# Kernel optimization log

Measured on AMD Instinct MI355X. Metric: run time of the kernel, lower is better.

## Reference

```python
import jax, jax.numpy as jnp
import numpy as np

B, L_I, L_H, L_Q, Hs, Ws, K, A = 256, 2, 150, 10, 128, 128, 40, 5


def _conv(x, w, pad):
    # NCHW conv, stride 1
    return jax.lax.conv_general_dilated(
        x, w, window_strides=(1, 1), padding=[(pad, pad), (pad, pad)],
        dimension_numbers=('NCHW', 'OIHW', 'NCHW'))


def setup_inputs() -> dict:
    key = jax.random.key(0)
    ks = jax.random.split(key, 8)
    return {
        'input_view': jax.random.normal(ks[0], (B, L_I, Hs, Ws), dtype=jnp.float32),
        'coords': jax.random.randint(ks[1], (B, 4), 0, Hs, dtype=jnp.int32),
        'h_w': jax.random.normal(ks[2], (L_H, L_I, 3, 3), dtype=jnp.float32) * 0.05,
        'h_b': jax.random.normal(ks[3], (L_H,), dtype=jnp.float32) * 0.05,
        'r_w': jax.random.normal(ks[4], (1, L_H, 1, 1), dtype=jnp.float32) * 0.05,
        'q_w': jax.random.normal(ks[5], (L_Q, 1, 3, 3), dtype=jnp.float32) * 0.05,
        'w': jax.random.normal(ks[6], (L_Q, 1, 3, 3), dtype=jnp.float32) * 0.05,
        'fc_w': jax.random.normal(ks[7], (A, L_Q), dtype=jnp.float32) * 0.05,
    }


def reference(input_view, coords, h_w, h_b, r_w, q_w, w, fc_w):
    # process_input: h = Conv3x3(input_view), r = Conv1x1(h), q0 = Conv3x3(r)
    h = _conv(input_view, h_w, pad=1) + h_b[None, :, None, None]
    r = _conv(h, r_w, pad=0)                       # [B,1,H,W] reward map
    q = _conv(r, q_w, pad=1)                       # [B,L_Q,H,W]
    v = jnp.max(q, axis=1, keepdims=True)          # [B,1,H,W]

    # value_iteration: k-1 sweeps of eval_q + channel max, then one final eval_q
    wq = jnp.concatenate([q_w, w], axis=1)         # [L_Q,2,3,3]

    def step(_, v):
        q_i = _conv(jnp.concatenate([r, v], axis=1), wq, pad=1)
        return jnp.max(q_i, axis=1, keepdims=True)

    v = jax.lax.fori_loop(0, K - 1, step, v)
    q = _conv(jnp.concatenate([r, v], axis=1), wq, pad=1)  # [B,L_Q,H,W]

    # get_action: gather q at agent state, then fc (no bias)
    sx, sy = coords[:, 0], coords[:, 1]
    q_out = q[jnp.arange(B), :, sx, sy]            # [B,L_Q]
    logits = q_out @ fc_w.T                        # [B,5]
    return logits
```

## Files before the change

kernel.cpp:

```cpp
#include <hip/hip_runtime.h>

#define NBATCH 256
#define LI 2
#define LH 150
#define LQ 10
#define HS 128
#define WSD 128
#define KIT 40
#define AOUT 5

#define LCOLS 132
#define LROWS 130
#define PLANE (LROWS * LCOLS)
#define LDS_DWORDS (2 * PLANE)

#define WSOFF_RPLANES 64
#define WS_NEED_BYTES ((size_t)(WSOFF_RPLANES + NBATCH * PLANE) * 4)

typedef float v2f __attribute__((ext_vector_type(2)));
#define SPLAT(K) ((v2f){(K), (K)})
#define FMA2(A, B, C) __builtin_elementwise_fma((A), (B), (C))

__global__ void prep_weff(const float* __restrict__ h_w,
                          const float* __restrict__ h_b,
                          const float* __restrict__ r_w,
                          float* __restrict__ w_eff) {
  const int t = threadIdx.x;
  if (t < 18) {
    const int i = t / 9, k = t % 9;
    double s = 0.0;
    for (int h = 0; h < LH; ++h)
      s += (double)r_w[h] * (double)h_w[(h * LI + i) * 9 + k];
    w_eff[t] = (float)s;
  } else if (t == 18) {
    double s = 0.0;
    for (int h = 0; h < LH; ++h)
      s += (double)r_w[h] * (double)h_b[h];
    w_eff[18] = (float)s;
  }
}


#define LOAD_PROW(P, R, W)                                                   \
  {                                                                          \
    const float4 b_ = *reinterpret_cast<const float4*>((P) + (R) * LCOLS);   \
    const float2 c_ = *reinterpret_cast<const float2*>((P) + (R) * LCOLS + 4); \
    W[0] = (v2f){b_.x, b_.y};                                                \
    W[1] = (v2f){b_.z, b_.w};                                                \
    W[2] = (v2f){c_.x, c_.y};                                                \
  }

#define TAPROW(KY, WARR, K0, K1, K2)                                         \
    a0 = FMA2(SPLAT(K0), WARR[KY][0], a0);                                   \
    a1 = FMA2(SPLAT(K0), WARR[KY][1], a1);                                   \
    a0.x = __builtin_fmaf((K1), WARR[KY][0].y, a0.x);                        \
    a0.y = __builtin_fmaf((K1), WARR[KY][1].x, a0.y);                        \
    a1.x = __builtin_fmaf((K1), WARR[KY][1].y, a1.x);                        \
    a1.y = __builtin_fmaf((K1), WARR[KY][2].x, a1.y);                        \
    a0 = FMA2(SPLAT(K2), WARR[KY][1], a0);                                   \
    a1 = FMA2(SPLAT(K2), WARR[KY][2], a1);

#define VI_CH(QC, WC, MERGE)                                                 \
  {                                                                          \
    const float* qc = (QC);                                                  \
    const float* wc = (WC);                                                  \
    v2f a0 = SPLAT(qc[0]) * rw[0][0];                                        \
    v2f a1 = SPLAT(qc[0]) * rw[0][1];                                        \
    a0.x = __builtin_fmaf(qc[1], rw[0][0].y, a0.x);                          \
    a0.y = __builtin_fmaf(qc[1], rw[0][1].x, a0.y);                          \
    a1.x = __builtin_fmaf(qc[1], rw[0][1].y, a1.x);                          \
    a1.y = __builtin_fmaf(qc[1], rw[0][2].x, a1.y);                          \
    a0 = FMA2(SPLAT(qc[2]), rw[0][1], a0);                                   \
    a1 = FMA2(SPLAT(qc[2]), rw[0][2], a1);                                   \
    TAPROW(1, rw, qc[3], qc[4], qc[5])                                       \
    TAPROW(2, rw, qc[6], qc[7], qc[8])                                       \
    TAPROW(0, vw, wc[0], wc[1], wc[2])                                       \
    TAPROW(1, vw, wc[3], wc[4], wc[5])                                       \
    TAPROW(2, vw, wc[6], wc[7], wc[8])                                       \
    MERGE                                                                    \
  }

#define VI_CHANNELS                                                          \
    v2f o0, o1;                                                              \
    VI_CH(q_w, w_in, o0 = a0; o1 = a1;)                                      \
    _Pragma("unroll 3")                                                      \
    for (int c = 1; c < LQ; ++c) {                                           \
      VI_CH(q_w + c * 9, w_in + c * 9,                                       \
            o0 = __builtin_elementwise_max(o0, a0);                          \
            o1 = __builtin_elementwise_max(o1, a1);)                         \
    }

#define VI_ROW_L(DY)                                                         \
  {                                                                          \
    VI_CHANNELS                                                              \
    outv[DY][0] = o0; outv[DY][1] = o1;                                      \
  }

#define WIN_SHIFT2(NEXTROW)                                                  \
  {                                                                          \
    _Pragma("unroll")                                                        \
    for (int j = 0; j < 3; ++j) {                                            \
      rw[0][j] = rw[1][j]; rw[1][j] = rw[2][j];                              \
      vw[0][j] = vw[1][j]; vw[1][j] = vw[2][j];                              \
    }                                                                        \
    LOAD_PROW(rp, (NEXTROW), rw[2])                                          \
    LOAD_PROW(vp, (NEXTROW), vw[2])                                          \
  }

#define R_ROW(DY)                                                            \
  {                                                                          \
    v2f a0 = SPLAT(beff);                                                    \
    v2f a1 = a0;                                                             \
    TAPROW(0, rw, w_eff[0], w_eff[1], w_eff[2])                              \
    TAPROW(1, rw, w_eff[3], w_eff[4], w_eff[5])                              \
    TAPROW(2, rw, w_eff[6], w_eff[7], w_eff[8])                              \
    TAPROW(0, vw, w_eff[9], w_eff[10], w_eff[11])                            \
    TAPROW(1, vw, w_eff[12], w_eff[13], w_eff[14])                           \
    TAPROW(2, vw, w_eff[15], w_eff[16], w_eff[17])                           \
    racc[DY][0] = a0; racc[DY][1] = a1;                                      \
  }

#define LOADR(SLOT, R)                                                       \
  {                                                                          \
    const float4 b_ = *reinterpret_cast<const float4*>(rp + (R) * LCOLS);    \
    const float2 c_ = *reinterpret_cast<const float2*>(rp + (R) * LCOLS + 4); \
    rP[SLOT][0] = (v2f){b_.x, b_.y};                                         \
    rP[SLOT][1] = (v2f){b_.z, b_.w};                                         \
    rP[SLOT][2] = (v2f){c_.x, c_.y};                                         \
  }

#define LOADV(SLOT, R)                                                       \
  {                                                                          \
    const float4 b_ = *reinterpret_cast<const float4*>(vp + (R) * LCOLS);    \
    const float2 c_ = *reinterpret_cast<const float2*>(vp + (R) * LCOLS + 4); \
    vE[SLOT][0] = (v2f){b_.x, b_.y};                                         \
    vE[SLOT][1] = (v2f){b_.z, b_.w};                                         \
    vE[SLOT][2] = (v2f){c_.x, c_.y};                                         \
    vO[SLOT][0] = (v2f){b_.y, b_.z};                                         \
    vO[SLOT][1] = (v2f){b_.w, c_.x};                                         \
  }

#define TAP_R(SLOT, K0, K1, K2)                                              \
    a0 = FMA2(SPLAT(K0), rP[SLOT][0], a0);                                   \
    a1 = FMA2(SPLAT(K0), rP[SLOT][1], a1);                                   \
    a0.x = __builtin_fmaf((K1), rP[SLOT][0].y, a0.x);                        \
    a0.y = __builtin_fmaf((K1), rP[SLOT][1].x, a0.y);                        \
    a1.x = __builtin_fmaf((K1), rP[SLOT][1].y, a1.x);                        \
    a1.y = __builtin_fmaf((K1), rP[SLOT][2].x, a1.y);                        \
    a0 = FMA2(SPLAT(K2), rP[SLOT][1], a0);                                   \
    a1 = FMA2(SPLAT(K2), rP[SLOT][2], a1);

#define TAP_V(SLOT, K0, K1, K2)                                              \
    a0 = FMA2(SPLAT(K0), vE[SLOT][0], a0);                                   \
    a1 = FMA2(SPLAT(K0), vE[SLOT][1], a1);                                   \
    a0 = FMA2(SPLAT(K1), vO[SLOT][0], a0);                                   \
    a1 = FMA2(SPLAT(K1), vO[SLOT][1], a1);                                   \
    a0 = FMA2(SPLAT(K2), vE[SLOT][1], a0);                                   \
    a1 = FMA2(SPLAT(K2), vE[SLOT][2], a1);

#define VI_CH3(QC, WC, SA, SB, SC, MERGE)                                    \
  {                                                                          \
    const float* qc = (QC);                                                  \
    const float* wc = (WC);                                                  \
    v2f a0 = SPLAT(qc[0]) * rP[SA][0];                                       \
    v2f a1 = SPLAT(qc[0]) * rP[SA][1];                                       \
    a0.x = __builtin_fmaf(qc[1], rP[SA][0].y, a0.x);                         \
    a0.y = __builtin_fmaf(qc[1], rP[SA][1].x, a0.y);                         \
    a1.x = __builtin_fmaf(qc[1], rP[SA][1].y, a1.x);                         \
    a1.y = __builtin_fmaf(qc[1], rP[SA][2].x, a1.y);                         \
    a0 = FMA2(SPLAT(qc[2]), rP[SA][1], a0);                                  \
    a1 = FMA2(SPLAT(qc[2]), rP[SA][2], a1);                                  \
    TAP_R(SB, qc[3], qc[4], qc[5])                                           \
    TAP_R(SC, qc[6], qc[7], qc[8])                                           \
    TAP_V(SA, wc[0], wc[1], wc[2])                                           \
    TAP_V(SB, wc[3], wc[4], wc[5])                                           \
    TAP_V(SC, wc[6], wc[7], wc[8])                                           \
    MERGE                                                                    \
  }

#define VI_OUT(DY, SA, SB, SC)                                               \
  {                                                                          \
    v2f o0, o1;                                                              \
    VI_CH3(q_w, w_in, SA, SB, SC, o0 = a0; o1 = a1;)                         \
    _Pragma("unroll 3")                                                      \
    for (int c = 1; c < LQ; ++c) {                                           \
      VI_CH3(q_w + c * 9, w_in + c * 9, SA, SB, SC,                          \
             o0 = __builtin_elementwise_max(o0, a0);                         \
             o1 = __builtin_elementwise_max(o1, a1);)                        \
    }                                                                        \
    float* w_ = wr + (DY) * LCOLS;                                           \
    w_[1] = o0.x; w_[2] = o0.y; w_[3] = o1.x; w_[4] = o1.y;                  \
  }

__global__ __launch_bounds__(1024)
__attribute__((amdgpu_waves_per_eu(4, 4)))
void vin_gr(const float* __restrict__ input,
            const int* __restrict__ coords,
            const float* __restrict__ q_w,
            const float* __restrict__ w_in,
            const float* __restrict__ fc_w,
            float* __restrict__ ws,
            float* __restrict__ out) {
  extern __shared__ float lds[];
  float* pA = lds;
  float* pB = lds + PLANE;
  const float* w_eff = ws;
  float* g_r = ws + WSOFF_RPLANES + (size_t)blockIdx.x * PLANE;

  const int b = blockIdx.x;
  const int tid = threadIdx.x;
  const int ty = tid >> 5;
  const int tx = tid & 31;
  const int y0 = ty << 2;
  const int x0 = tx << 2;
  const int nb_base = y0 * LCOLS + x0;
  const int wrow0 = (y0 + 1) * LCOLS + x0;

  for (int i = tid; i < LDS_DWORDS; i += 1024) lds[i] = 0.0f;
  if (tid < LCOLS) { g_r[tid] = 0.0f; g_r[129 * LCOLS + tid] = 0.0f; }
  if (tid >= 256 && tid < 384) {
    const int row = tid - 255;
    g_r[row * LCOLS + 0] = 0.0f;
    g_r[row * LCOLS + 129] = 0.0f;
    g_r[row * LCOLS + 130] = 0.0f;
    g_r[row * LCOLS + 131] = 0.0f;
  }
  __syncthreads();

  const float* in0 = input + (size_t)b * (LI * HS * WSD);
  const float* in1 = in0 + HS * WSD;
  {
    const float4* in40 = (const float4*)in0;
    const float4* in41 = (const float4*)in1;
    for (int i = tid; i < HS * WSD / 4; i += 1024) {
      const int y = i >> 5, x4 = (i & 31) << 2;
      const float4 a = in40[i];
      const float4 c = in41[i];
      float* r_ = pA + (y + 1) * LCOLS + x4;
      float* v_ = pB + (y + 1) * LCOLS + x4;
      r_[1] = a.x; r_[2] = a.y; r_[3] = a.z; r_[4] = a.w;
      v_[1] = c.x; v_[2] = c.y; v_[3] = c.z; v_[4] = c.w;
    }
  }
  __syncthreads();

  {
    const float* rp = pA + nb_base;
    const float* vp = pB + nb_base;
    v2f rw[3][3], vw[3][3], racc[4][2];
    LOAD_PROW(rp, 0, rw[0]) LOAD_PROW(rp, 1, rw[1]) LOAD_PROW(rp, 2, rw[2])
    LOAD_PROW(vp, 0, vw[0]) LOAD_PROW(vp, 1, vw[1]) LOAD_PROW(vp, 2, vw[2])
    const float beff = w_eff[18];
    R_ROW(0) WIN_SHIFT2(3) R_ROW(1) WIN_SHIFT2(4) R_ROW(2) WIN_SHIFT2(5) R_ROW(3)
    __syncthreads();
#pragma unroll
    for (int dy = 0; dy < 4; ++dy) {
      float* g_ = g_r + wrow0 + dy * LCOLS;
      float* v_ = pA + wrow0 + dy * LCOLS;
      g_[1] = racc[dy][0].x; g_[2] = racc[dy][0].y;
      g_[3] = racc[dy][1].x; g_[4] = racc[dy][1].y;
      v_[1] = 0.0f; v_[2] = 0.0f; v_[3] = 0.0f; v_[4] = 0.0f;
    }
  }
  __syncthreads();

  const float* grp = g_r + nb_base;
#pragma unroll 1
  for (int it = 0; it < KIT; ++it) {
    const float* vp = lds + ((it & 1) ? PLANE : 0) + nb_base;
    float* wr = lds + ((it & 1) ? 0 : PLANE) + wrow0;
    const float* rp = grp;
    v2f rP[3][3], vE[3][3], vO[3][2];
    LOADR(0, 0) LOADR(1, 1) LOADR(2, 2)
    LOADV(0, 0) LOADV(1, 1) LOADV(2, 2)
    VI_OUT(0, 0, 1, 2)
    LOADR(0, 3) LOADV(0, 3)
    VI_OUT(1, 1, 2, 0)
    LOADR(1, 4) LOADV(1, 4)
    VI_OUT(2, 2, 0, 1)
    LOADR(2, 5) LOADV(2, 5)
    VI_OUT(3, 0, 1, 2)
    __syncthreads();
  }

  if (tid == 0) {
    const int sx = coords[b * 4 + 0];
    const int sy = coords[b * 4 + 1];
    float qv[LQ];
#pragma unroll 1
    for (int c = 0; c < LQ; ++c) {
      float s = 0.0f;
#pragma unroll
      for (int kk = 0; kk < 9; ++kk) {
        const int ky = kk / 3, kx = kk % 3;
        const int off = (sx + ky) * LCOLS + (sy + kx);
        s = __builtin_fmaf(q_w[c * 9 + kk], g_r[off],
            __builtin_fmaf(w_in[c * 9 + kk], pA[off], s));
      }
      qv[c] = s;
    }
#pragma unroll 1
    for (int a = 0; a < AOUT; ++a) {
      float s = 0.0f;
#pragma unroll
      for (int c = 0; c < LQ; ++c)
        s = __builtin_fmaf(fc_w[a * LQ + c], qv[c], s);
      out[b * AOUT + a] = s;
    }
  }
}

__global__ __launch_bounds__(1024)
__attribute__((amdgpu_waves_per_eu(4, 4)))
void vin_lds(const float* __restrict__ input,
             const int* __restrict__ coords,
             const float* __restrict__ q_w,
             const float* __restrict__ w_in,
             const float* __restrict__ fc_w,
             const float* __restrict__ w_eff,
             float* __restrict__ out) {
  extern __shared__ float lds[];
  float* rplane = lds;
  float* vplane = lds + PLANE;

  const int b = blockIdx.x;
  const int tid = threadIdx.x;
  const int ty = tid >> 5;
  const int tx = tid & 31;
  const int y0 = ty << 2;
  const int x0 = tx << 2;
  const int nb_base = y0 * LCOLS + x0;
  const int wrow0 = (y0 + 1) * LCOLS + x0;

  for (int i = tid; i < LDS_DWORDS; i += 1024) lds[i] = 0.0f;
  __syncthreads();

  const float* in0 = input + (size_t)b * (LI * HS * WSD);
  const float* in1 = in0 + HS * WSD;
  {
    const float4* in40 = (const float4*)in0;
    const float4* in41 = (const float4*)in1;
    for (int i = tid; i < HS * WSD / 4; i += 1024) {
      const int y = i >> 5, x4 = (i & 31) << 2;
      const float4 a = in40[i];
      const float4 c = in41[i];
      float* r_ = rplane + (y + 1) * LCOLS + x4;
      float* v_ = vplane + (y + 1) * LCOLS + x4;
      r_[1] = a.x; r_[2] = a.y; r_[3] = a.z; r_[4] = a.w;
      v_[1] = c.x; v_[2] = c.y; v_[3] = c.z; v_[4] = c.w;
    }
  }
  __syncthreads();

  {
    const float* rp = rplane + nb_base;
    const float* vp = vplane + nb_base;
    v2f rw[3][3], vw[3][3], racc[4][2];
    LOAD_PROW(rp, 0, rw[0]) LOAD_PROW(rp, 1, rw[1]) LOAD_PROW(rp, 2, rw[2])
    LOAD_PROW(vp, 0, vw[0]) LOAD_PROW(vp, 1, vw[1]) LOAD_PROW(vp, 2, vw[2])
    const float beff = w_eff[18];
    R_ROW(0) WIN_SHIFT2(3) R_ROW(1) WIN_SHIFT2(4) R_ROW(2) WIN_SHIFT2(5) R_ROW(3)
    __syncthreads();
#pragma unroll
    for (int dy = 0; dy < 4; ++dy) {
      float* r_ = rplane + wrow0 + dy * LCOLS;
      float* v_ = vplane + wrow0 + dy * LCOLS;
      r_[1] = racc[dy][0].x; r_[2] = racc[dy][0].y;
      r_[3] = racc[dy][1].x; r_[4] = racc[dy][1].y;
      v_[1] = 0.0f; v_[2] = 0.0f; v_[3] = 0.0f; v_[4] = 0.0f;
    }
  }
  __syncthreads();

#pragma unroll 1
  for (int it = 0; it < KIT; ++it) {
    const float* rp = rplane + nb_base;
    const float* vp = vplane + nb_base;
    v2f rw[3][3], vw[3][3], outv[4][2];
    LOAD_PROW(rp, 0, rw[0]) LOAD_PROW(rp, 1, rw[1]) LOAD_PROW(rp, 2, rw[2])
    LOAD_PROW(vp, 0, vw[0]) LOAD_PROW(vp, 1, vw[1]) LOAD_PROW(vp, 2, vw[2])
    VI_ROW_L(0) WIN_SHIFT2(3) VI_ROW_L(1) WIN_SHIFT2(4) VI_ROW_L(2) WIN_SHIFT2(5) VI_ROW_L(3)
    __syncthreads();
#pragma unroll
    for (int dy = 0; dy < 4; ++dy) {
      float* v_ = vplane + wrow0 + dy * LCOLS;
      v_[1] = outv[dy][0].x; v_[2] = outv[dy][0].y;
      v_[3] = outv[dy][1].x; v_[4] = outv[dy][1].y;
    }
    __syncthreads();
  }

  if (tid == 0) {
    const int sx = coords[b * 4 + 0];
    const int sy = coords[b * 4 + 1];
    float qv[LQ];
#pragma unroll 1
    for (int c = 0; c < LQ; ++c) {
      float s = 0.0f;
#pragma unroll
      for (int kk = 0; kk < 9; ++kk) {
        const int ky = kk / 3, kx = kk % 3;
        const int off = (sx + ky) * LCOLS + (sy + kx);
        s = __builtin_fmaf(q_w[c * 9 + kk], rplane[off],
            __builtin_fmaf(w_in[c * 9 + kk], vplane[off], s));
      }
      qv[c] = s;
    }
#pragma unroll 1
    for (int a = 0; a < AOUT; ++a) {
      float s = 0.0f;
#pragma unroll
      for (int c = 0; c < LQ; ++c)
        s = __builtin_fmaf(fc_w[a * LQ + c], qv[c], s);
      out[b * AOUT + a] = s;
    }
  }
}

extern "C" void kernel_launch(void* const* d_in, const int* in_sizes, int n_in,
                              void* d_out, int out_size, void* d_ws, size_t ws_size,
                              hipStream_t stream) {
  const float* input = (const float*)d_in[0];
  const int*   coords = (const int*)d_in[1];
  const float* h_w = (const float*)d_in[2];
  const float* h_b = (const float*)d_in[3];
  const float* r_w = (const float*)d_in[4];
  const float* q_w = (const float*)d_in[5];
  const float* w_in = (const float*)d_in[6];
  const float* fc_w = (const float*)d_in[7];
  float* out = (float*)d_out;
  float* ws = (float*)d_ws;

  const size_t smem = (size_t)LDS_DWORDS * sizeof(float);

  prep_weff<<<1, 64, 0, stream>>>(h_w, h_b, r_w, ws);

  if (ws_size >= WS_NEED_BYTES) {
    hipFuncSetAttribute(reinterpret_cast<const void*>(vin_gr),
                        hipFuncAttributeMaxDynamicSharedMemorySize, (int)smem);
    vin_gr<<<NBATCH, 1024, smem, stream>>>(input, coords, q_w, w_in, fc_w, ws, out);
  } else {
    hipFuncSetAttribute(reinterpret_cast<const void*>(vin_lds),
                        hipFuncAttributeMaxDynamicSharedMemorySize, (int)smem);
    vin_lds<<<NBATCH, 1024, smem, stream>>>(input, coords, q_w, w_in, fc_w, ws, out);
  }
}
```

Measured before the change: 642.2 us.

## Precompute loop-invariant reward-conv term per channel and double-buffer value planes

Adds a new kernel that computes the reward-map half of the value-iteration conv (q_w applied to r) once per channel and pixel and stores it in global workspace. Each of the 40 iterations then only convolves the value plane with w and adds the stored term, which removes about half the FMAs per iteration. The value plane is ping-ponged between two LDS buffers, so one barrier per iteration replaces two. In exchange every iteration reads 40 float4 per thread from global/L2 (about 640KB per block, 160MB total workspace), which could become memory-bound. The old pure-LDS fallback kernel is removed.

```diff
diff --git a/kernel.cpp b/kernel.cpp
--- a/kernel.cpp
+++ b/kernel.cpp
@@ -14,8 +14,10 @@
 #define PLANE (LROWS * LCOLS)
 #define LDS_DWORDS (2 * PLANE)
 
-#define WSOFF_RPLANES 64
-#define WS_NEED_BYTES ((size_t)(WSOFF_RPLANES + NBATCH * PLANE) * 4)
+#define WSOFF 64
+#define QR_BLOCK_DW (LQ * 4 * 1024 * 4)
+#define WS_QR_BYTES ((size_t)(WSOFF + (size_t)NBATCH * QR_BLOCK_DW) * 4)
+#define WS_GR_BYTES ((size_t)(WSOFF + (size_t)NBATCH * PLANE) * 4)
 
 typedef float v2f __attribute__((ext_vector_type(2)));
 #define SPLAT(K) ((v2f){(K), (K)})
@@ -60,42 +62,6 @@
     a0 = FMA2(SPLAT(K2), WARR[KY][1], a0);                                   \
     a1 = FMA2(SPLAT(K2), WARR[KY][2], a1);
 
-#define VI_CH(QC, WC, MERGE)                                                 \
-  {                                                                          \
-    const float* qc = (QC);                                                  \
-    const float* wc = (WC);                                                  \
-    v2f a0 = SPLAT(qc[0]) * rw[0][0];                                        \
-    v2f a1 = SPLAT(qc[0]) * rw[0][1];                                        \
-    a0.x = __builtin_fmaf(qc[1], rw[0][0].y, a0.x);                          \
-    a0.y = __builtin_fmaf(qc[1], rw[0][1].x, a0.y);                          \
-    a1.x = __builtin_fmaf(qc[1], rw[0][1].y, a1.x);                          \
-    a1.y = __builtin_fmaf(qc[1], rw[0][2].x, a1.y);                          \
-    a0 = FMA2(SPLAT(qc[2]), rw[0][1], a0);                                   \
-    a1 = FMA2(SPLAT(qc[2]), rw[0][2], a1);                                   \
-    TAPROW(1, rw, qc[3], qc[4], qc[5])                                       \
-    TAPROW(2, rw, qc[6], qc[7], qc[8])                                       \
-    TAPROW(0, vw, wc[0], wc[1], wc[2])                                       \
-    TAPROW(1, vw, wc[3], wc[4], wc[5])                                       \
-    TAPROW(2, vw, wc[6], wc[7], wc[8])                                       \
-    MERGE                                                                    \
-  }
-
-#define VI_CHANNELS                                                          \
-    v2f o0, o1;                                                              \
-    VI_CH(q_w, w_in, o0 = a0; o1 = a1;)                                      \
-    _Pragma("unroll 3")                                                      \
-    for (int c = 1; c < LQ; ++c) {                                           \
-      VI_CH(q_w + c * 9, w_in + c * 9,                                       \
-            o0 = __builtin_elementwise_max(o0, a0);                          \
-            o1 = __builtin_elementwise_max(o1, a1);)                         \
-    }
-
-#define VI_ROW_L(DY)                                                         \
-  {                                                                          \
-    VI_CHANNELS                                                              \
-    outv[DY][0] = o0; outv[DY][1] = o1;                                      \
-  }
-
 #define WIN_SHIFT2(NEXTROW)                                                  \
   {                                                                          \
     _Pragma("unroll")                                                        \
@@ -120,15 +86,6 @@
     racc[DY][0] = a0; racc[DY][1] = a1;                                      \
   }
 
-#define LOADR(SLOT, R)                                                       \
-  {                                                                          \
-    const float4 b_ = *reinterpret_cast<const float4*>(rp + (R) * LCOLS);    \
-    const float2 c_ = *reinterpret_cast<const float2*>(rp + (R) * LCOLS + 4); \
-    rP[SLOT][0] = (v2f){b_.x, b_.y};                                         \
-    rP[SLOT][1] = (v2f){b_.z, b_.w};                                         \
-    rP[SLOT][2] = (v2f){c_.x, c_.y};                                         \
-  }
-
 #define LOADV(SLOT, R)                                                       \
   {                                                                          \
     const float4 b_ = *reinterpret_cast<const float4*>(vp + (R) * LCOLS);    \
@@ -138,6 +95,217 @@
     vE[SLOT][2] = (v2f){c_.x, c_.y};                                         \
     vO[SLOT][0] = (v2f){b_.y, b_.z};                                         \
     vO[SLOT][1] = (v2f){b_.w, c_.x};                                         \
+  }
+
+#define TAP_V(SLOT, K0, K1, K2)                                              \
+    a0 = FMA2(SPLAT(K0), vE[SLOT][0], a0);                                   \
+    a1 = FMA2(SPLAT(K0), vE[SLOT][1], a1);                                   \
+    a0 = FMA2(SPLAT(K1), vO[SLOT][0], a0);                                   \
+    a1 = FMA2(SPLAT(K1), vO[SLOT][1], a1);                                   \
+    a0 = FMA2(SPLAT(K2), vE[SLOT][1], a0);                                   \
+    a1 = FMA2(SPLAT(K2), vE[SLOT][2], a1);
+
+#define TAP_VS(SLOT, K0, K1, K2)                                             \
+    a0 = SPLAT(K0) * vE[SLOT][0];                                            \
+    a1 = SPLAT(K0) * vE[SLOT][1];                                            \
+    a0 = FMA2(SPLAT(K1), vO[SLOT][0], a0);                                   \
+    a1 = FMA2(SPLAT(K1), vO[SLOT][1], a1);                                   \
+    a0 = FMA2(SPLAT(K2), vE[SLOT][1], a0);                                   \
+    a1 = FMA2(SPLAT(K2), vE[SLOT][2], a1);
+
+#define VQ_CH(C_, DY, SA, SB, SC, MERGE)                                     \
+  {                                                                          \
+    const float* wc = w_in + (C_) * 9;                                       \
+    const float4 qf = qr4[((C_) * 4 + (DY)) * 1024 + tid];                   \
+    v2f a0, a1;                                                              \
+    TAP_VS(SA, wc[0], wc[1], wc[2])                                          \
+    TAP_V(SB, wc[3], wc[4], wc[5])                                           \
+    TAP_V(SC, wc[6], wc[7], wc[8])                                           \
+    a0 += (v2f){qf.x, qf.y};                                                 \
+    a1 += (v2f){qf.z, qf.w};                                                 \
+    MERGE                                                                    \
+  }
+
+#define VI_OUT_Q(DY, SA, SB, SC)                                             \
+  {                                                                          \
+    v2f o0, o1;                                                              \
+    VQ_CH(0, DY, SA, SB, SC, o0 = a0; o1 = a1;)                              \
+    _Pragma("unroll 2")                                                      \
+    for (int c = 1; c < LQ; ++c) {                                           \
+      VQ_CH(c, DY, SA, SB, SC,                                               \
+            o0 = __builtin_elementwise_max(o0, a0);                          \
+            o1 = __builtin_elementwise_max(o1, a1);)                         \
+    }                                                                        \
+    float* w_ = wr + (DY) * LCOLS;                                           \
+    w_[1] = o0.x; w_[2] = o0.y; w_[3] = o1.x; w_[4] = o1.y;                  \
+  }
+
+#define LOADR2(SLOT, R)                                                      \
+  {                                                                          \
+    const float4 b_ = *reinterpret_cast<const float4*>(rp + (R) * LCOLS);    \
+    const float2 c_ = *reinterpret_cast<const float2*>(rp + (R) * LCOLS + 4); \
+    rE[SLOT][0] = (v2f){b_.x, b_.y};                                         \
+    rE[SLOT][1] = (v2f){b_.z, b_.w};                                         \
+    rE[SLOT][2] = (v2f){c_.x, c_.y};                                         \
+    rO[SLOT][0] = (v2f){b_.y, b_.z};                                         \
+    rO[SLOT][1] = (v2f){b_.w, c_.x};                                         \
+  }
+
+#define QTAP(SLOT, K0, K1, K2)                                               \
+    a0 = FMA2(SPLAT(K0), rE[SLOT][0], a0);                                   \
+    a1 = FMA2(SPLAT(K0), rE[SLOT][1], a1);                                   \
+    a0 = FMA2(SPLAT(K1), rO[SLOT][0], a0);                                   \
+    a1 = FMA2(SPLAT(K1), rO[SLOT][1], a1);                                   \
+    a0 = FMA2(SPLAT(K2), rE[SLOT][1], a0);                                   \
+    a1 = FMA2(SPLAT(K2), rE[SLOT][2], a1);
+
+#define QTAP_S(SLOT, K0, K1, K2)                                             \
+    a0 = SPLAT(K0) * rE[SLOT][0];                                            \
+    a1 = SPLAT(K0) * rE[SLOT][1];                                            \
+    a0 = FMA2(SPLAT(K1), rO[SLOT][0], a0);                                   \
+    a1 = FMA2(SPLAT(K1), rO[SLOT][1], a1);                                   \
+    a0 = FMA2(SPLAT(K2), rE[SLOT][1], a0);                                   \
+    a1 = FMA2(SPLAT(K2), rE[SLOT][2], a1);
+
+#define QR_ROW(DY, SA, SB, SC)                                               \
+  {                                                                          \
+    _Pragma("unroll 2")                                                      \
+    for (int c = 0; c < LQ; ++c) {                                           \
+      const float* qc = q_w + c * 9;                                         \
+      v2f a0, a1;                                                            \
+      QTAP_S(SA, qc[0], qc[1], qc[2])                                        \
+      QTAP(SB, qc[3], qc[4], qc[5])                                          \
+      QTAP(SC, qc[6], qc[7], qc[8])                                          \
+      qr4[(c * 4 + (DY)) * 1024 + tid] =                                     \
+          make_float4(a0.x, a0.y, a1.x, a1.y);                               \
+    }                                                                        \
+  }
+
+__global__ __launch_bounds__(1024)
+__attribute__((amdgpu_waves_per_eu(4, 4)))
+void vin_qr(const float* __restrict__ input,
+            const int* __restrict__ coords,
+            const float* __restrict__ q_w,
+            const float* __restrict__ w_in,
+            const float* __restrict__ fc_w,
+            float* __restrict__ ws,
+            float* __restrict__ out) {
+  extern __shared__ float lds[];
+  float* pA = lds;
+  float* pB = lds + PLANE;
+  const float* w_eff = ws;
+  float4* qr4 = reinterpret_cast<float4*>(ws + WSOFF) +
+                (size_t)blockIdx.x * (QR_BLOCK_DW / 4);
+
+  const int b = blockIdx.x;
+  const int tid = threadIdx.x;
+  const int ty = tid >> 5;
+  const int tx = tid & 31;
+  const int y0 = ty << 2;
+  const int x0 = tx << 2;
+  const int nb_base = y0 * LCOLS + x0;
+  const int wrow0 = (y0 + 1) * LCOLS + x0;
+
+  for (int i = tid; i < LDS_DWORDS; i += 1024) lds[i] = 0.0f;
+  __syncthreads();
+
+  const float* in0 = input + (size_t)b * (LI * HS * WSD);
+  const float* in1 = in0 + HS * WSD;
+  {
+    const float4* in40 = (const float4*)in0;
+    const float4* in41 = (const float4*)in1;
+    for (int i = tid; i < HS * WSD / 4; i += 1024) {
+      const int y = i >> 5, x4 = (i & 31) << 2;
+      const float4 a = in40[i];
+      const float4 c = in41[i];
+      float* r_ = pA + (y + 1) * LCOLS + x4;
+      float* v_ = pB + (y + 1) * LCOLS + x4;
+      r_[1] = a.x; r_[2] = a.y; r_[3] = a.z; r_[4] = a.w;
+      v_[1] = c.x; v_[2] = c.y; v_[3] = c.z; v_[4] = c.w;
+    }
+  }
+  __syncthreads();
+
+  {
+    const float* rp = pA + nb_base;
+    const float* vp = pB + nb_base;
+    v2f rw[3][3], vw[3][3], racc[4][2];
+    LOAD_PROW(rp, 0, rw[0]) LOAD_PROW(rp, 1, rw[1]) LOAD_PROW(rp, 2, rw[2])
+    LOAD_PROW(vp, 0, vw[0]) LOAD_PROW(vp, 1, vw[1]) LOAD_PROW(vp, 2, vw[2])
+    const float beff = w_eff[18];
+    R_ROW(0) WIN_SHIFT2(3) R_ROW(1) WIN_SHIFT2(4) R_ROW(2) WIN_SHIFT2(5) R_ROW(3)
+    __syncthreads();
+#pragma unroll
+    for (int dy = 0; dy < 4; ++dy) {
+      float* r_ = pA + wrow0 + dy * LCOLS;
+      float* v_ = pB + wrow0 + dy * LCOLS;
+      r_[1] = racc[dy][0].x; r_[2] = racc[dy][0].y;
+      r_[3] = racc[dy][1].x; r_[4] = racc[dy][1].y;
+      v_[1] = 0.0f; v_[2] = 0.0f; v_[3] = 0.0f; v_[4] = 0.0f;
+    }
+  }
+  __syncthreads();
+
+  {
+    const float* rp = pA + nb_base;
+    v2f rE[3][3], rO[3][2];
+    LOADR2(0, 0) LOADR2(1, 1) LOADR2(2, 2)
+    QR_ROW(0, 0, 1, 2)
+    LOADR2(0, 3) QR_ROW(1, 1, 2, 0)
+    LOADR2(1, 4) QR_ROW(2, 2, 0, 1)
+    LOADR2(2, 5) QR_ROW(3, 0, 1, 2)
+  }
+  __syncthreads();
+
+#pragma unroll 1
+  for (int it = 0; it < KIT; ++it) {
+    const float* vp = lds + ((it & 1) ? 0 : PLANE) + nb_base;
+    float* wr = lds + ((it & 1) ? PLANE : 0) + wrow0;
+    v2f vE[3][3], vO[3][2];
+    LOADV(0, 0) LOADV(1, 1) LOADV(2, 2)
+    VI_OUT_Q(0, 0, 1, 2)
+    LOADV(0, 3) VI_OUT_Q(1, 1, 2, 0)
+    LOADV(1, 4) VI_OUT_Q(2, 2, 0, 1)
+    LOADV(2, 5) VI_OUT_Q(3, 0, 1, 2)
+    __syncthreads();
+  }
+
+  if (tid == 0) {
+    const int sx = coords[b * 4 + 0];
+    const int sy = coords[b * 4 + 1];
+    const float* qrf = reinterpret_cast<const float*>(qr4);
+    const int tidp = ((sx >> 2) << 5) | (sy >> 2);
+    const int dyp = sx & 3, pxp = sy & 3;
+    float qv[LQ];
+#pragma unroll 1
+    for (int c = 0; c < LQ; ++c) {
+      float s = qrf[((c * 4 + dyp) * 1024 + tidp) * 4 + pxp];
+#pragma unroll
+      for (int kk = 0; kk < 9; ++kk) {
+        const int ky = kk / 3, kx = kk % 3;
+        s = __builtin_fmaf(w_in[c * 9 + kk],
+                           pB[(sx + ky) * LCOLS + (sy + kx)], s);
+      }
+      qv[c] = s;
+    }
+#pragma unroll 1
+    for (int a = 0; a < AOUT; ++a) {
+      float s = 0.0f;
+#pragma unroll
+      for (int c = 0; c < LQ; ++c)
+        s = __builtin_fmaf(fc_w[a * LQ + c], qv[c], s);
+      out[b * AOUT + a] = s;
+    }
+  }
+}
+
+#define LOADR(SLOT, R)                                                       \
+  {                                                                          \
+    const float4 b_ = *reinterpret_cast<const float4*>(rp + (R) * LCOLS);    \
+    const float2 c_ = *reinterpret_cast<const float2*>(rp + (R) * LCOLS + 4); \
+    rP[SLOT][0] = (v2f){b_.x, b_.y};                                         \
+    rP[SLOT][1] = (v2f){b_.z, b_.w};                                         \
+    rP[SLOT][2] = (v2f){c_.x, c_.y};                                         \
   }
 
 #define TAP_R(SLOT, K0, K1, K2)                                              \
@@ -149,14 +317,6 @@
     a1.y = __builtin_fmaf((K1), rP[SLOT][2].x, a1.y);                        \
     a0 = FMA2(SPLAT(K2), rP[SLOT][1], a0);                                   \
     a1 = FMA2(SPLAT(K2), rP[SLOT][2], a1);
-
-#define TAP_V(SLOT, K0, K1, K2)                                              \
-    a0 = FMA2(SPLAT(K0), vE[SLOT][0], a0);                                   \
-    a1 = FMA2(SPLAT(K0), vE[SLOT][1], a1);                                   \
-    a0 = FMA2(SPLAT(K1), vO[SLOT][0], a0);                                   \
-    a1 = FMA2(SPLAT(K1), vO[SLOT][1], a1);                                   \
-    a0 = FMA2(SPLAT(K2), vE[SLOT][1], a0);                                   \
-    a1 = FMA2(SPLAT(K2), vE[SLOT][2], a1);
 
 #define VI_CH3(QC, WC, SA, SB, SC, MERGE)                                    \
   {                                                                          \
@@ -205,7 +365,7 @@
   float* pA = lds;
   float* pB = lds + PLANE;
   const float* w_eff = ws;
-  float* g_r = ws + WSOFF_RPLANES + (size_t)blockIdx.x * PLANE;
+  float* g_r = ws + WSOFF + (size_t)blockIdx.x * PLANE;
 
   const int b = blockIdx.x;
   const int tid = threadIdx.x;
@@ -310,113 +470,6 @@
   }
 }
 
-__global__ __launch_bounds__(1024)
-__attribute__((amdgpu_waves_per_eu(4, 4)))
-void vin_lds(const float* __restrict__ input,
-             const int* __restrict__ coords,
-             const float* __restrict__ q_w,
-             const float* __restrict__ w_in,
-             const float* __restrict__ fc_w,
-             const float* __restrict__ w_eff,
-             float* __restrict__ out) {
-  extern __shared__ float lds[];
-  float* rplane = lds;
-  float* vplane = lds + PLANE;
-
-  const int b = blockIdx.x;
-  const int tid = threadIdx.x;
-  const int ty = tid >> 5;
-  const int tx = tid & 31;
-  const int y0 = ty << 2;
-  const int x0 = tx << 2;
-  const int nb_base = y0 * LCOLS + x0;
-  const int wrow0 = (y0 + 1) * LCOLS + x0;
-
-  for (int i = tid; i < LDS_DWORDS; i += 1024) lds[i] = 0.0f;
-  __syncthreads();
-
-  const float* in0 = input + (size_t)b * (LI * HS * WSD);
-  const float* in1 = in0 + HS * WSD;
-  {
-    const float4* in40 = (const float4*)in0;
-    const float4* in41 = (const float4*)in1;
-    for (int i = tid; i < HS * WSD / 4; i += 1024) {
-      const int y = i >> 5, x4 = (i & 31) << 2;
-      const float4 a = in40[i];
-      const float4 c = in41[i];
-      float* r_ = rplane + (y + 1) * LCOLS + x4;
-      float* v_ = vplane + (y + 1) * LCOLS + x4;
-      r_[1] = a.x; r_[2] = a.y; r_[3] = a.z; r_[4] = a.w;
-      v_[1] = c.x; v_[2] = c.y; v_[3] = c.z; v_[4] = c.w;
-    }
-  }
-  __syncthreads();
-
-  {
-    const float* rp = rplane + nb_base;
-    const float* vp = vplane + nb_base;
-    v2f rw[3][3], vw[3][3], racc[4][2];
-    LOAD_PROW(rp, 0, rw[0]) LOAD_PROW(rp, 1, rw[1]) LOAD_PROW(rp, 2, rw[2])
-    LOAD_PROW(vp, 0, vw[0]) LOAD_PROW(vp, 1, vw[1]) LOAD_PROW(vp, 2, vw[2])
-    const float beff = w_eff[18];
-    R_ROW(0) WIN_SHIFT2(3) R_ROW(1) WIN_SHIFT2(4) R_ROW(2) WIN_SHIFT2(5) R_ROW(3)
-    __syncthreads();
-#pragma unroll
-    for (int dy = 0; dy < 4; ++dy) {
-      float* r_ = rplane + wrow0 + dy * LCOLS;
-      float* v_ = vplane + wrow0 + dy * LCOLS;
-      r_[1] = racc[dy][0].x; r_[2] = racc[dy][0].y;
-      r_[3] = racc[dy][1].x; r_[4] = racc[dy][1].y;
-      v_[1] = 0.0f; v_[2] = 0.0f; v_[3] = 0.0f; v_[4] = 0.0f;
-    }
-  }
-  __syncthreads();
-
-#pragma unroll 1
-  for (int it = 0; it < KIT; ++it) {
-    const float* rp = rplane + nb_base;
-    const float* vp = vplane + nb_base;
-    v2f rw[3][3], vw[3][3], outv[4][2];
-    LOAD_PROW(rp, 0, rw[0]) LOAD_PROW(rp, 1, rw[1]) LOAD_PROW(rp, 2, rw[2])
-    LOAD_PROW(vp, 0, vw[0]) LOAD_PROW(vp, 1, vw[1]) LOAD_PROW(vp, 2, vw[2])
-    VI_ROW_L(0) WIN_SHIFT2(3) VI_ROW_L(1) WIN_SHIFT2(4) VI_ROW_L(2) WIN_SHIFT2(5) VI_ROW_L(3)
-    __syncthreads();
-#pragma unroll
-    for (int dy = 0; dy < 4; ++dy) {
-      float* v_ = vplane + wrow0 + dy * LCOLS;
-      v_[1] = outv[dy][0].x; v_[2] = outv[dy][0].y;
-      v_[3] = outv[dy][1].x; v_[4] = outv[dy][1].y;
-    }
-    __syncthreads();
-  }
-
-  if (tid == 0) {
-    const int sx = coords[b * 4 + 0];
-    const int sy = coords[b * 4 + 1];
-    float qv[LQ];
-#pragma unroll 1
-    for (int c = 0; c < LQ; ++c) {
-      float s = 0.0f;
-#pragma unroll
-      for (int kk = 0; kk < 9; ++kk) {
-        const int ky = kk / 3, kx = kk % 3;
-        const int off = (sx + ky) * LCOLS + (sy + kx);
-        s = __builtin_fmaf(q_w[c * 9 + kk], rplane[off],
-            __builtin_fmaf(w_in[c * 9 + kk], vplane[off], s));
-      }
-      qv[c] = s;
-    }
-#pragma unroll 1
-    for (int a = 0; a < AOUT; ++a) {
-      float s = 0.0f;
-#pragma unroll
-      for (int c = 0; c < LQ; ++c)
-        s = __builtin_fmaf(fc_w[a * LQ + c], qv[c], s);
-      out[b * AOUT + a] = s;
-    }
-  }
-}
-
 extern "C" void kernel_launch(void* const* d_in, const int* in_sizes, int n_in,
                               void* d_out, int out_size, void* d_ws, size_t ws_size,
                               hipStream_t stream) {
@@ -435,13 +488,13 @@
 
   prep_weff<<<1, 64, 0, stream>>>(h_w, h_b, r_w, ws);
 
-  if (ws_size >= WS_NEED_BYTES) {
+  if (ws_size >= WS_QR_BYTES) {
+    hipFuncSetAttribute(reinterpret_cast<const void*>(vin_qr),
+                        hipFuncAttributeMaxDynamicSharedMemorySize, (int)smem);
+    vin_qr<<<NBATCH, 1024, smem, stream>>>(input, coords, q_w, w_in, fc_w, ws, out);
+  } else {
     hipFuncSetAttribute(reinterpret_cast<const void*>(vin_gr),
                         hipFuncAttributeMaxDynamicSharedMemorySize, (int)smem);
     vin_gr<<<NBATCH, 1024, smem, stream>>>(input, coords, q_w, w_in, fc_w, ws, out);
-  } else {
-    hipFuncSetAttribute(reinterpret_cast<const void*>(vin_lds),
-                        hipFuncAttributeMaxDynamicSharedMemorySize, (int)smem);
-    vin_lds<<<NBATCH, 1024, smem, stream>>>(input, coords, q_w, w_in, fc_w, ws, out);
   }
 }
```

Result: slower. 972.9 us (+51.5%).
